# Kernel tuning notes

Measured on AMD Instinct MI355X. Metric: run time of the kernel, lower is better.

## Reference

```python
import jax, jax.numpy as jnp
import numpy as np

DIM = 1024
H = 16          # query heads
HKV = 4         # kv heads
HD = DIM // H   # head_dim = 64
B = 8           # equal-length docs
S = 1024        # tokens per doc
N = B * S       # total tokens
ROPE_BASE = 10000.0


def _rms_norm(x, scale):
    eps = jnp.asarray(jnp.finfo(x.dtype).eps, x.dtype)
    inv = jax.lax.rsqrt(jnp.mean(x * x, axis=-1, keepdims=True) + eps)
    return x * inv * scale


def _rope(x, cos, sin):
    # x: [N, h, HD]; cos/sin: [N, 1, HD//2]
    half = x.shape[-1] // 2
    x1, x2 = x[..., :half], x[..., half:]
    return jnp.concatenate((x1 * cos + x2 * sin, -x1 * sin + x2 * cos), axis=-1)


def setup_inputs() -> dict:
    key = jax.random.key(0)
    ks = jax.random.split(key, 8)
    x = jax.random.normal(ks[0], (N, DIM), dtype=jnp.float32)
    Wq = jax.random.normal(ks[1], (DIM, DIM), dtype=jnp.float32) * (DIM ** -0.5)
    Wk = jax.random.normal(ks[2], (HKV * HD, DIM), dtype=jnp.float32) * (DIM ** -0.5)
    Wv = jax.random.normal(ks[3], (HKV * HD, DIM), dtype=jnp.float32) * (DIM ** -0.5)
    Wproj = jax.random.normal(ks[4], (DIM, DIM), dtype=jnp.float32) * (DIM ** -0.5)
    q_gain = jnp.full((H,), 1.0, dtype=jnp.float32)
    q_scale = jnp.asarray(1.0, dtype=jnp.float32)  # q RMSNorm scale
    k_scale = jnp.asarray(1.0, dtype=jnp.float32)  # k RMSNorm scale
    # rotary tables per Rotary.prepare_positions (positions reset per doc)
    cu_seqlens = jnp.arange(B + 1, dtype=jnp.int32) * S
    positions = jnp.tile(jnp.arange(S, dtype=jnp.float32), B)  # [N]
    inv_freq = 1.0 / (ROPE_BASE ** (jnp.arange(0, HD, 2, dtype=jnp.float32) / HD))
    freqs = positions[:, None] * inv_freq[None, :]  # [N, HD//2]
    rotary_cos = jnp.cos(freqs)[:, None, :]
    rotary_sin = jnp.sin(freqs)[:, None, :]
    return {
        "x": x, "Wq": Wq, "Wk": Wk, "Wv": Wv, "Wproj": Wproj,
        "q_gain": q_gain, "q_scale": q_scale, "k_scale": k_scale,
        "rotary_cos": rotary_cos, "rotary_sin": rotary_sin,
        "cu_seqlens": cu_seqlens, "max_doc_len": S,
    }


def reference(x, Wq, Wk, Wv, Wproj, q_gain, q_scale, k_scale,
              rotary_cos, rotary_sin, cu_seqlens, max_doc_len):
    n_tokens, dim = x.shape
    q = (x @ Wq.T).reshape(n_tokens, H, HD)
    k = (x @ Wk.T).reshape(n_tokens, HKV, HD)
    v = (x @ Wv.T).reshape(n_tokens, HKV, HD)
    q = _rms_norm(q, q_scale)
    k = _rms_norm(k, k_scale)
    q = _rope(q, rotary_cos, rotary_sin)
    k = _rope(k, rotary_cos, rotary_sin)
    q = q * q_gain[None, :, None]
    # equal-length docs -> [B, S, h, HD]; GQA: repeat kv heads
    rep = H // HKV
    qb = q.reshape(B, S, H, HD)
    kb = jnp.repeat(k.reshape(B, S, HKV, HD), rep, axis=2)
    vb = jnp.repeat(v.reshape(B, S, HKV, HD), rep, axis=2)
    scale = HD ** -0.5
    scores = jnp.einsum('bqhd,bkhd->bhqk', qb, kb) * scale  # [B,H,S,S]
    causal = jnp.tril(jnp.ones((S, S), dtype=bool))
    scores = jnp.where(causal[None, None], scores, jnp.asarray(-jnp.inf, scores.dtype))
    attn = jax.nn.softmax(scores, axis=-1)
    y = jnp.einsum('bhqk,bkhd->bqhd', attn, vb).reshape(n_tokens, dim)
    return y @ Wproj.T
```

## Files before the change

kernel.cpp:

```cpp
#include <hip/hip_runtime.h>
#include <hip/hip_bf16.h>


typedef __bf16 bf16x8 __attribute__((ext_vector_type(8)));
typedef float f32x4 __attribute__((ext_vector_type(4)));

__device__ __forceinline__ void async16(const void* g, void* l) {
  __builtin_amdgcn_global_load_lds((const __attribute__((address_space(1))) void*)g,
                                   (__attribute__((address_space(3))) void*)l, 16, 0, 0);
}

__device__ __forceinline__ unsigned short f2bfu(float x) {
  __hip_bfloat16 h = __float2bfloat16(x);
  return __builtin_bit_cast(unsigned short, h);
}

__global__ __launch_bounds__(256) void castall(
    const float4* __restrict__ x, const float4* __restrict__ Wq,
    const float4* __restrict__ Wk, const float4* __restrict__ Wv,
    const float4* __restrict__ Wp,
    ushort4* __restrict__ xb, ushort4* __restrict__ w1b, ushort4* __restrict__ wpb) {
  int i = blockIdx.x * 256 + threadIdx.x;
  const float4* src;
  ushort4* dst;
  if (i < 2097152)      { src = x + i;             dst = xb + i; }
  else if (i < 2359296) { src = Wq + (i - 2097152); dst = w1b + (i - 2097152); }
  else if (i < 2424832) { src = Wk + (i - 2359296); dst = w1b + (i - 2097152); }
  else if (i < 2490368) { src = Wv + (i - 2424832); dst = w1b + (i - 2097152); }
  else                  { src = Wp + (i - 2490368); dst = wpb + (i - 2490368); }
  float4 v = *src;
  ushort4 o;
  o.x = f2bfu(v.x); o.y = f2bfu(v.y); o.z = f2bfu(v.z); o.w = f2bfu(v.w);
  *dst = o;
}

__global__ __launch_bounds__(256, 4) void gemm_qkv(
    const __hip_bfloat16* __restrict__ A,
    const __hip_bfloat16* __restrict__ Bm,
    const float* __restrict__ cosb, const float* __restrict__ sinb,
    const float* __restrict__ qgain, const float* __restrict__ qscale,
    const float* __restrict__ kscale,
    __hip_bfloat16* __restrict__ Qo,
    __hip_bfloat16* __restrict__ Ko,
    __hip_bfloat16* __restrict__ Vt)
{
  __shared__ __align__(16) unsigned short As[128 * 64];
  __shared__ __align__(16) unsigned short Bs[128 * 64];
  const int tid = threadIdx.x;
  const int wave = tid >> 6, lane = tid & 63;
  const int quad = lane >> 4, l15 = lane & 15;
  const int flat = blockIdx.x;
  const int swz = (flat & 7) * 96 + (flat >> 3);
  const int bn = swz % 12, bm = swz / 12;
  const int wm = (wave >> 1) * 64, wn = (wave & 1) * 64;
  const int srow = lane >> 3;
  const int scol = ((lane & 7) ^ srow) * 8;
  const int K = 1024;

  f32x4 acc[4][4] = {};

  const __hip_bfloat16* Ab = A + (size_t)bm * 128 * K;
  const __hip_bfloat16* Bb = Bm + (size_t)bn * 128 * K;

  for (int kt = 0; kt < K; kt += 64) {
    __syncthreads();
#pragma unroll
    for (int c = 0; c < 4; c++) {
      const int ch = wave * 4 + c;
      async16(Ab + (size_t)(ch * 8 + srow) * K + kt + scol, &As[ch * 512]);
      async16(Bb + (size_t)(ch * 8 + srow) * K + kt + scol, &Bs[ch * 512]);
    }
    __syncthreads();
#pragma unroll
    for (int ks = 0; ks < 2; ks++) {
      bf16x8 af[4], bfr[4];
#pragma unroll
      for (int mt = 0; mt < 4; mt++) {
        const int row = wm + mt * 16 + l15;
        af[mt] = *(const bf16x8*)&As[row * 64 + (((ks << 2) + quad) ^ (row & 7)) * 8];
      }
#pragma unroll
      for (int nt = 0; nt < 4; nt++) {
        const int row = wn + nt * 16 + l15;
        bfr[nt] = *(const bf16x8*)&Bs[row * 64 + (((ks << 2) + quad) ^ (row & 7)) * 8];
      }
#pragma unroll
      for (int mt = 0; mt < 4; mt++)
#pragma unroll
        for (int nt = 0; nt < 4; nt++)
          acc[mt][nt] = __builtin_amdgcn_mfma_f32_16x16x32_bf16(af[mt], bfr[nt], acc[mt][nt], 0, 0, 0);
    }
  }

  const int hg = bn * 2 + (wn >> 6);
  const int tokbase = bm * 128 + wm;

  if (hg >= 20) {
    const int hv = hg - 20;
    const int bb = tokbase >> 10;
    const int s0 = tokbase & 1023;
    unsigned short* vt = (unsigned short*)Vt + ((size_t)(bb * 4 + hv) * 64) * 1024;
#pragma unroll
    for (int mt = 0; mt < 4; mt++)
#pragma unroll
      for (int r = 0; r < 4; r++) {
        const int so = s0 + mt * 16 + quad * 4 + r;
#pragma unroll
        for (int nt = 0; nt < 4; nt++)
          vt[(size_t)(nt * 16 + l15) * 1024 + so] = f2bfu(acc[mt][nt][r]);
      }
  } else {
    const bool isq = hg < 16;
    const float scale = isq ? qscale[0] : kscale[0];
    const float gain = isq ? qgain[hg] * 0.18033688011112042f : 1.0f;
    const float sg = scale * gain;
#pragma unroll
    for (int mt = 0; mt < 4; mt++) {
      float inv[4];
#pragma unroll
      for (int r = 0; r < 4; r++) {
        float ss = acc[mt][0][r] * acc[mt][0][r] + acc[mt][1][r] * acc[mt][1][r] +
                   acc[mt][2][r] * acc[mt][2][r] + acc[mt][3][r] * acc[mt][3][r];
#pragma unroll
        for (int off = 1; off < 16; off <<= 1) ss += __shfl_xor(ss, off);
        inv[r] = rsqrtf(ss * (1.0f / 64.0f) + 1.1920929e-07f) * sg;
      }
#pragma unroll
      for (int r = 0; r < 4; r++) {
        const int tok = tokbase + mt * 16 + quad * 4 + r;
        const float c0 = cosb[tok * 32 + l15], c1 = cosb[tok * 32 + 16 + l15];
        const float s0 = sinb[tok * 32 + l15], s1 = sinb[tok * 32 + 16 + l15];
        const float v0 = acc[mt][0][r] * inv[r];
        const float v1 = acc[mt][1][r] * inv[r];
        const float v2 = acc[mt][2][r] * inv[r];
        const float v3 = acc[mt][3][r] * inv[r];
        const float o0 = v0 * c0 + v2 * s0;
        const float o1 = v1 * c1 + v3 * s1;
        const float o2 = -v0 * s0 + v2 * c0;
        const float o3 = -v1 * s1 + v3 * c1;
        __hip_bfloat16* base = isq ? (Qo + (size_t)tok * 1024 + hg * 64)
                                   : (Ko + (size_t)tok * 256 + (hg - 16) * 64);
        base[l15]      = __float2bfloat16(o0);
        base[16 + l15] = __float2bfloat16(o1);
        base[32 + l15] = __float2bfloat16(o2);
        base[48 + l15] = __float2bfloat16(o3);
      }
    }
  }
}

__global__ __launch_bounds__(256, 4) void gemm_p(
    const __hip_bfloat16* __restrict__ A,
    const __hip_bfloat16* __restrict__ Bm,
    float* __restrict__ C)
{
  __shared__ __align__(16) unsigned short As[128 * 64];
  __shared__ __align__(16) unsigned short Bs[128 * 64];
  const int tid = threadIdx.x;
  const int wave = tid >> 6, lane = tid & 63;
  const int quad = lane >> 4, l15 = lane & 15;
  const int flat = blockIdx.x;
  const int swz = (flat & 7) * 64 + (flat >> 3);
  const int bn = swz & 7, bm = swz >> 3;
  const int wm = (wave >> 1) * 64, wn = (wave & 1) * 64;
  const int srow = lane >> 3;
  const int scol = ((lane & 7) ^ srow) * 8;
  const int K = 1024;

  f32x4 acc[4][4] = {};

  const __hip_bfloat16* Ab = A + (size_t)bm * 128 * K;
  const __hip_bfloat16* Bb = Bm + (size_t)bn * 128 * K;

  for (int kt = 0; kt < K; kt += 64) {
    __syncthreads();
#pragma unroll
    for (int c = 0; c < 4; c++) {
      const int ch = wave * 4 + c;
      async16(Ab + (size_t)(ch * 8 + srow) * K + kt + scol, &As[ch * 512]);
      async16(Bb + (size_t)(ch * 8 + srow) * K + kt + scol, &Bs[ch * 512]);
    }
    __syncthreads();
#pragma unroll
    for (int ks = 0; ks < 2; ks++) {
      bf16x8 af[4], bfr[4];
#pragma unroll
      for (int mt = 0; mt < 4; mt++) {
        const int row = wm + mt * 16 + l15;
        af[mt] = *(const bf16x8*)&As[row * 64 + (((ks << 2) + quad) ^ (row & 7)) * 8];
      }
#pragma unroll
      for (int nt = 0; nt < 4; nt++) {
        const int row = wn + nt * 16 + l15;
        bfr[nt] = *(const bf16x8*)&Bs[row * 64 + (((ks << 2) + quad) ^ (row & 7)) * 8];
      }
#pragma unroll
      for (int mt = 0; mt < 4; mt++)
#pragma unroll
        for (int nt = 0; nt < 4; nt++)
          acc[mt][nt] = __builtin_amdgcn_mfma_f32_16x16x32_bf16(af[mt], bfr[nt], acc[mt][nt], 0, 0, 0);
    }
  }

#pragma unroll
  for (int mt = 0; mt < 4; mt++)
#pragma unroll
    for (int r = 0; r < 4; r++) {
      const int row = bm * 128 + wm + mt * 16 + quad * 4 + r;
#pragma unroll
      for (int nt = 0; nt < 4; nt++)
        C[(size_t)row * 1024 + bn * 128 + wn + nt * 16 + l15] = acc[mt][nt][r];
    }
}

__global__ __launch_bounds__(256, 2) void attn(
    const __hip_bfloat16* __restrict__ Q,
    const __hip_bfloat16* __restrict__ Kk,
    const __hip_bfloat16* __restrict__ Vt,
    __hip_bfloat16* __restrict__ Y)
{
  __shared__ __align__(16) unsigned short Kb[2][4096];
  __shared__ __align__(16) unsigned short Vb[2][4096];
  __shared__ __align__(16) unsigned short Pm[4][2048];

  const int p = blockIdx.x;
  const int qt_a = 15 - p, qt_b = p;
  const int kvh2 = blockIdx.y;
  const int kvh = kvh2 >> 1, hh = kvh2 & 1;
  const int b = blockIdx.z;
  const int tid = threadIdx.x;
  const int wave = tid >> 6, lane = tid & 63;
  const int quad = lane >> 4, l15 = lane & 15;
  const int h = kvh * 4 + hh * 2 + (wave >> 1);
  const int m0 = (wave & 1) * 32;
  const int sr8 = lane >> 3;
  const int sc8 = ((lane & 7) ^ sr8) * 8;

  auto issue = [&](int kt, unsigned short* Ks, unsigned short* Vs) {
#pragma unroll
    for (int c = 0; c < 4; c++) {
      const int ch = wave * 4 + c;
      const int g8 = ch & 7;
      if (ch < 8)
        async16(Kk + (size_t)(b * 1024 + kt * 64 + g8 * 8 + sr8) * 256 + kvh * 64 + sc8,
                Ks + g8 * 512 + lane * 8);
      else
        async16(Vt + ((size_t)((b * 4 + kvh) * 64 + g8 * 8 + sr8)) * 1024 + kt * 64 + sc8,
                Vs + g8 * 512 + lane * 8);
    }
  };

  bf16x8 qf[2][2];
  {
    const int tok0 = b * 1024 + qt_a * 64;
#pragma unroll
    for (int mt = 0; mt < 2; mt++)
#pragma unroll
      for (int kc = 0; kc < 2; kc++)
        qf[mt][kc] = *(const bf16x8*)(Q + (size_t)(tok0 + m0 + mt * 16 + l15) * 1024 +
                                      h * 64 + kc * 32 + quad * 8);
  }

  issue(0, Kb[0], Vb[0]);

  f32x4 of[2][4] = {};
  f32x4 lf[2] = {};
  unsigned short* Pw = Pm[wave];

  bf16x8 onesf;
#pragma unroll
  for (int j = 0; j < 8; j++) onesf[j] = (__bf16)1.0f;

  const int steps_a = qt_a + 1;
  const int total = steps_a + qt_b + 1;

  for (int g = 0; g < total; ++g) {
    const bool pa = g < steps_a;
    const int qtc = pa ? qt_a : qt_b;
    const int kt = pa ? g : g - steps_a;

    __syncthreads();
    if (g + 1 < total) {
      const int gn = g + 1;
      const int ktn = (gn < steps_a) ? gn : gn - steps_a;
      issue(ktn, Kb[gn & 1], Vb[gn & 1]);
    }
    if (g == steps_a) {
      const int tok0 = b * 1024 + qt_b * 64;
#pragma unroll
      for (int mt = 0; mt < 2; mt++)
#pragma unroll
        for (int kc = 0; kc < 2; kc++)
          qf[mt][kc] = *(const bf16x8*)(Q + (size_t)(tok0 + m0 + mt * 16 + l15) * 1024 +
                                        h * 64 + kc * 32 + quad * 8);
    }
    const unsigned short* Ks = Kb[g & 1];
    const unsigned short* Vs = Vb[g & 1];

    f32x4 sf[4][2] = {};
    __builtin_amdgcn_s_setprio(1);
#pragma unroll
    for (int kc = 0; kc < 2; kc++) {
#pragma unroll
      for (int kk = 0; kk < 4; kk++) {
        const int krow = kk * 16 + l15;
        const bf16x8 kf = *(const bf16x8*)&Ks[krow * 64 + (((kc * 4 + quad) ^ (krow & 7)) * 8)];
#pragma unroll
        for (int mt = 0; mt < 2; mt++)
          sf[kk][mt] = __builtin_amdgcn_mfma_f32_16x16x32_bf16(kf, qf[mt][kc], sf[kk][mt], 0, 0, 0);
      }
    }
    __builtin_amdgcn_s_setprio(0);

    const bool diag = (kt == qtc);
#pragma unroll
    for (int mt = 0; mt < 2; mt++) {
      const int prow = mt * 16 + l15;
#pragma unroll
      for (int kk = 0; kk < 4; kk++) {
        ushort4 pk;
        unsigned short* pp = (unsigned short*)&pk;
#pragma unroll
        for (int r = 0; r < 4; r++) {
          float pv;
          if (diag && (kk * 16 + quad * 4 + r) > (m0 + mt * 16 + l15))
            pv = 0.0f;
          else
            pv = __builtin_amdgcn_exp2f(sf[kk][mt][r]);
          pp[r] = f2bfu(pv);
        }
        const int b8 = kk * 2 + (quad >> 1);
        *(ushort4*)&Pw[prow * 64 + ((b8 ^ (prow & 7)) * 8) + (quad & 1) * 4] = pk;
      }
    }

    asm volatile("s_waitcnt lgkmcnt(0)" ::: "memory");

    __builtin_amdgcn_s_setprio(1);
#pragma unroll
    for (int kc = 0; kc < 2; kc++) {
      bf16x8 bv[4];
#pragma unroll
      for (int dt = 0; dt < 4; dt++) {
        const int vrow = dt * 16 + l15;
        bv[dt] = *(const bf16x8*)&Vs[vrow * 64 + (((kc * 4 + quad) ^ (vrow & 7)) * 8)];
      }
#pragma unroll
      for (int mt = 0; mt < 2; mt++) {
        const int prow = mt * 16 + l15;
        const bf16x8 ap = *(const bf16x8*)&Pw[prow * 64 + (((kc * 4 + quad) ^ (prow & 7)) * 8)];
        lf[mt] = __builtin_amdgcn_mfma_f32_16x16x32_bf16(ap, onesf, lf[mt], 0, 0, 0);
#pragma unroll
        for (int dt = 0; dt < 4; dt++)
          of[mt][dt] = __builtin_amdgcn_mfma_f32_16x16x32_bf16(ap, bv[dt], of[mt][dt], 0, 0, 0);
      }
    }
    __builtin_amdgcn_s_setprio(0);

    if (diag) {
      const int tok0 = b * 1024 + qtc * 64;
#pragma unroll
      for (int mt = 0; mt < 2; mt++)
#pragma unroll
        for (int r = 0; r < 4; r++) {
          const float rcp = 1.0f / lf[mt][r];
          const int row = tok0 + m0 + mt * 16 + quad * 4 + r;
#pragma unroll
          for (int dt = 0; dt < 4; dt++)
            Y[(size_t)row * 1024 + h * 64 + dt * 16 + l15] = __float2bfloat16(of[mt][dt][r] * rcp);
        }
      if (pa) {
#pragma unroll
        for (int mt = 0; mt < 2; mt++) {
          lf[mt] = f32x4{0.f, 0.f, 0.f, 0.f};
#pragma unroll
          for (int dt = 0; dt < 4; dt++) of[mt][dt] = f32x4{0.f, 0.f, 0.f, 0.f};
        }
      }
    }
  }
}

extern "C" void kernel_launch(void* const* d_in, const int* in_sizes, int n_in,
                              void* d_out, int out_size, void* d_ws, size_t ws_size,
                              hipStream_t stream) {
  const float* x      = (const float*)d_in[0];
  const float* Wq     = (const float*)d_in[1];
  const float* Wk     = (const float*)d_in[2];
  const float* Wv     = (const float*)d_in[3];
  const float* Wp     = (const float*)d_in[4];
  const float* qgain  = (const float*)d_in[5];
  const float* qscale = (const float*)d_in[6];
  const float* kscale = (const float*)d_in[7];
  const float* cosb   = (const float*)d_in[8];
  const float* sinb   = (const float*)d_in[9];
  float* out = (float*)d_out;
  char* ws = (char*)d_ws;

  __hip_bfloat16* xb  = (__hip_bfloat16*)(ws);
  __hip_bfloat16* w1b = (__hip_bfloat16*)(ws + 16777216);
  __hip_bfloat16* wpb = (__hip_bfloat16*)(ws + 19922944);
  __hip_bfloat16* qb  = (__hip_bfloat16*)(ws + 22020096);
  __hip_bfloat16* kb  = (__hip_bfloat16*)(ws + 38797312);
  __hip_bfloat16* vtb = (__hip_bfloat16*)(ws + 47185920);
  __hip_bfloat16* yb  = (__hip_bfloat16*)(ws + 51380224);

  castall<<<10752, 256, 0, stream>>>((const float4*)x, (const float4*)Wq, (const float4*)Wk,
                                     (const float4*)Wv, (const float4*)Wp,
                                     (ushort4*)xb, (ushort4*)w1b, (ushort4*)wpb);

  gemm_qkv<<<768, 256, 0, stream>>>(xb, w1b, cosb, sinb, qgain, qscale, kscale,
                                    qb, kb, vtb);

  attn<<<dim3(8, 8, 8), 256, 0, stream>>>(qb, kb, vtb, yb);

  gemm_p<<<512, 256, 0, stream>>>(yb, wpb, out);
}
```

Baseline: 191.4 us.

## Split paired causal query tiles into one block per tile, raise occupancy

The attention kernel previously paired query tile 15-p with tile p in one block so every block did equal causal work. Now each block handles a single query tile, launched in heaviest-first order (qt = 15 - blockIdx.y) with the KV-head pair on the fastest grid axis, and the launch bound goes from 2 to 3 blocks per SM. This doubles the block count to 1024 and lets the hardware scheduler balance the uneven work, in exchange for losing the static pairing and accepting tighter register limits.

```diff
diff --git a/kernel.cpp b/kernel.cpp
--- a/kernel.cpp
+++ b/kernel.cpp
@@ -213,7 +213,7 @@
     }
 }
 
-__global__ __launch_bounds__(256, 2) void attn(
+__global__ __launch_bounds__(256, 3) void attn(
     const __hip_bfloat16* __restrict__ Q,
     const __hip_bfloat16* __restrict__ Kk,
     const __hip_bfloat16* __restrict__ Vt,
@@ -223,11 +223,10 @@
   __shared__ __align__(16) unsigned short Vb[2][4096];
   __shared__ __align__(16) unsigned short Pm[4][2048];
 
-  const int p = blockIdx.x;
-  const int qt_a = 15 - p, qt_b = p;
-  const int kvh2 = blockIdx.y;
+  const int kvh2 = blockIdx.x;
+  const int qt = 15 - blockIdx.y;
+  const int b = blockIdx.z;
   const int kvh = kvh2 >> 1, hh = kvh2 & 1;
-  const int b = blockIdx.z;
   const int tid = threadIdx.x;
   const int wave = tid >> 6, lane = tid & 63;
   const int quad = lane >> 4, l15 = lane & 15;
@@ -252,7 +251,7 @@
 
   bf16x8 qf[2][2];
   {
-    const int tok0 = b * 1024 + qt_a * 64;
+    const int tok0 = b * 1024 + qt * 64;
 #pragma unroll
     for (int mt = 0; mt < 2; mt++)
 #pragma unroll
@@ -271,31 +270,11 @@
 #pragma unroll
   for (int j = 0; j < 8; j++) onesf[j] = (__bf16)1.0f;
 
-  const int steps_a = qt_a + 1;
-  const int total = steps_a + qt_b + 1;
-
-  for (int g = 0; g < total; ++g) {
-    const bool pa = g < steps_a;
-    const int qtc = pa ? qt_a : qt_b;
-    const int kt = pa ? g : g - steps_a;
-
-    __syncthreads();
-    if (g + 1 < total) {
-      const int gn = g + 1;
-      const int ktn = (gn < steps_a) ? gn : gn - steps_a;
-      issue(ktn, Kb[gn & 1], Vb[gn & 1]);
-    }
-    if (g == steps_a) {
-      const int tok0 = b * 1024 + qt_b * 64;
-#pragma unroll
-      for (int mt = 0; mt < 2; mt++)
-#pragma unroll
-        for (int kc = 0; kc < 2; kc++)
-          qf[mt][kc] = *(const bf16x8*)(Q + (size_t)(tok0 + m0 + mt * 16 + l15) * 1024 +
-                                        h * 64 + kc * 32 + quad * 8);
-    }
-    const unsigned short* Ks = Kb[g & 1];
-    const unsigned short* Vs = Vb[g & 1];
+  for (int kt = 0; kt <= qt; ++kt) {
+    __syncthreads();
+    if (kt < qt) issue(kt + 1, Kb[(kt + 1) & 1], Vb[(kt + 1) & 1]);
+    const unsigned short* Ks = Kb[kt & 1];
+    const unsigned short* Vs = Vb[kt & 1];
 
     f32x4 sf[4][2] = {};
     __builtin_amdgcn_s_setprio(1);
@@ -312,7 +291,7 @@
     }
     __builtin_amdgcn_s_setprio(0);
 
-    const bool diag = (kt == qtc);
+    const bool diag = (kt == qt);
 #pragma unroll
     for (int mt = 0; mt < 2; mt++) {
       const int prow = mt * 16 + l15;
@@ -356,28 +335,20 @@
       }
     }
     __builtin_amdgcn_s_setprio(0);
-
-    if (diag) {
-      const int tok0 = b * 1024 + qtc * 64;
-#pragma unroll
-      for (int mt = 0; mt < 2; mt++)
-#pragma unroll
-        for (int r = 0; r < 4; r++) {
-          const float rcp = 1.0f / lf[mt][r];
-          const int row = tok0 + m0 + mt * 16 + quad * 4 + r;
-#pragma unroll
-          for (int dt = 0; dt < 4; dt++)
-            Y[(size_t)row * 1024 + h * 64 + dt * 16 + l15] = __float2bfloat16(of[mt][dt][r] * rcp);
-        }
-      if (pa) {
-#pragma unroll
-        for (int mt = 0; mt < 2; mt++) {
-          lf[mt] = f32x4{0.f, 0.f, 0.f, 0.f};
-#pragma unroll
-          for (int dt = 0; dt < 4; dt++) of[mt][dt] = f32x4{0.f, 0.f, 0.f, 0.f};
-        }
-      }
-    }
+  }
+
+  {
+    const int tok0 = b * 1024 + qt * 64;
+#pragma unroll
+    for (int mt = 0; mt < 2; mt++)
+#pragma unroll
+      for (int r = 0; r < 4; r++) {
+        const float rcp = 1.0f / lf[mt][r];
+        const int row = tok0 + m0 + mt * 16 + quad * 4 + r;
+#pragma unroll
+        for (int dt = 0; dt < 4; dt++)
+          Y[(size_t)row * 1024 + h * 64 + dt * 16 + l15] = __float2bfloat16(of[mt][dt][r] * rcp);
+      }
   }
 }
 
@@ -412,7 +383,7 @@
   gemm_qkv<<<768, 256, 0, stream>>>(xb, w1b, cosb, sinb, qgain, qscale, kscale,
                                     qb, kb, vtb);
 
-  attn<<<dim3(8, 8, 8), 256, 0, stream>>>(qb, kb, vtb, yb);
+  attn<<<dim3(8, 16, 8), 256, 0, stream>>>(qb, kb, vtb, yb);
 
   gemm_p<<<512, 256, 0, stream>>>(yb, wpb, out);
 }
```

New measurement: 202.7 us. +5.9%, slower.
